# Kernel optimization log

Hardware: AMD Instinct MI355X
Metric: run time of the kernel (lower is better)

## Reference

```python
import jax, jax.numpy as jnp
import numpy as np

NUM_HEADS = 16
HEAD_DIM = 64  # hidden 1024 / 16 heads


def setup_inputs() -> dict:
    key = jax.random.key(0)
    ks = jax.random.split(key, 4)
    B, S, D = 2, 2048, 1024
    scale = 1.0 / np.sqrt(D)
    return {
        "hidden_states": jax.random.normal(ks[0], (B, S, D), jnp.float32),
        "Wq": jax.random.normal(ks[1], (D, D), jnp.float32) * scale,
        "bq": jnp.zeros((D,), jnp.float32),
        "Wk": jax.random.normal(ks[2], (D, D), jnp.float32) * scale,
        "bk": jnp.zeros((D,), jnp.float32),
        "Wv": jax.random.normal(ks[3], (D, D), jnp.float32) * scale,
        "bv": jnp.zeros((D,), jnp.float32),
    }


def _split_heads(x):
    B, S, D = x.shape
    return x.reshape(B, S, NUM_HEADS, HEAD_DIM).transpose(0, 2, 1, 3)  # [B,H,S,dh]


def reference(hidden_states, Wq, bq, Wk, bk, Wv, bv):
    q = _split_heads(hidden_states @ Wq + bq)
    k = _split_heads(hidden_states @ Wk + bk)
    v = _split_heads(hidden_states @ Wv + bv)
    scores = jnp.einsum("bhqd,bhkd->bhqk", q, k) / jnp.sqrt(
        jnp.asarray(HEAD_DIM, hidden_states.dtype))
    probs = jax.nn.softmax(scores, axis=-1)  # dropout is identity in eval mode
    ctx = jnp.einsum("bhqk,bhkd->bhqd", probs, v)
    B, H, S, dh = ctx.shape
    return ctx.transpose(0, 2, 1, 3).reshape(B, S, H * dh)
```

## Files before the change

kernel.cpp:

```cpp
#include <hip/hip_runtime.h>
#include <hip/hip_bf16.h>


typedef __attribute__((ext_vector_type(8))) short bf16x8;
typedef __attribute__((ext_vector_type(4))) float f32x4;
typedef __attribute__((ext_vector_type(4))) int int4v;

#define MFMA16(A, B, C) __builtin_amdgcn_mfma_f32_16x16x32_bf16((A), (B), (C), 0, 0, 0)

#if __has_builtin(__builtin_amdgcn_exp2f)
#define EXP2(x) __builtin_amdgcn_exp2f(x)
#else
#define EXP2(x) exp2f(x)
#endif

static __device__ __forceinline__ unsigned short f2bf(float f) {
    union { float f; unsigned int u; } v;
    v.f = f;
    return (unsigned short)((v.u + 0x8000u) >> 16);
}

static __device__ __forceinline__ void gload_lds16(const void* g, void* l) {
    __builtin_amdgcn_global_load_lds(
        (const __attribute__((address_space(1))) void*)g,
        (__attribute__((address_space(3))) void*)l, 16, 0, 0);
}

__global__ __launch_bounds__(256) void cast_hs(const float* __restrict__ in,
                                               unsigned short* __restrict__ out) {
    const size_t flat = ((size_t)blockIdx.x * 256 + threadIdx.x) * 8;
    const int m = (int)(flat >> 10);
    const int k = (int)(flat & 1023);
    float4 a0 = *reinterpret_cast<const float4*>(in + flat);
    float4 a1 = *reinterpret_cast<const float4*>(in + flat + 4);
    unsigned short t[8];
    t[0] = f2bf(a0.x); t[1] = f2bf(a0.y); t[2] = f2bf(a0.z); t[3] = f2bf(a0.w);
    t[4] = f2bf(a1.x); t[5] = f2bf(a1.y); t[6] = f2bf(a1.z); t[7] = f2bf(a1.w);
    const int csw = (((k >> 3) & 7) ^ (m & 7)) << 3;
    *reinterpret_cast<int4v*>(out + (size_t)m * 1024 + (k & ~63) + csw) =
        *reinterpret_cast<int4v*>(t);
}

__global__ __launch_bounds__(256) void transpose_cast_w(
    const float* __restrict__ W0, const float* __restrict__ W1,
    const float* __restrict__ W2, unsigned short* __restrict__ Wt) {
    __shared__ float Ts[64][65];
    const float* W = (blockIdx.z == 0) ? W0 : (blockIdx.z == 1) ? W1 : W2;
    unsigned short* O = Wt + (size_t)blockIdx.z * 1048576;

    const int t  = threadIdx.x;
    const int k0 = blockIdx.y * 64;
    const int n0 = blockIdx.x * 64;

    {
        const int kr = t >> 2, nc = (t & 3) * 16;
        const float* p = W + (size_t)(k0 + kr) * 1024 + n0 + nc;
        float4 r0 = *reinterpret_cast<const float4*>(p);
        float4 r1 = *reinterpret_cast<const float4*>(p + 4);
        float4 r2 = *reinterpret_cast<const float4*>(p + 8);
        float4 r3 = *reinterpret_cast<const float4*>(p + 12);
        float* d = &Ts[kr][nc];
        d[0]=r0.x; d[1]=r0.y; d[2]=r0.z; d[3]=r0.w;
        d[4]=r1.x; d[5]=r1.y; d[6]=r1.z; d[7]=r1.w;
        d[8]=r2.x; d[9]=r2.y; d[10]=r2.z; d[11]=r2.w;
        d[12]=r3.x; d[13]=r3.y; d[14]=r3.z; d[15]=r3.w;
    }
    __syncthreads();
    {
        const int nr = t >> 2, kc = (t & 3) * 16;
        unsigned short tmp[16];
#pragma unroll
        for (int i = 0; i < 16; i++) tmp[i] = f2bf(Ts[kc + i][nr]);
        unsigned short* base = O + (size_t)(n0 + nr) * 1024 + k0;
        const int c0 = ((kc >> 3) ^ (nr & 7)) & 7;
        const int c1 = (((kc >> 3) + 1) ^ (nr & 7)) & 7;
        *reinterpret_cast<int4v*>(base + c0 * 8) = *reinterpret_cast<int4v*>(&tmp[0]);
        *reinterpret_cast<int4v*>(base + c1 * 8) = *reinterpret_cast<int4v*>(&tmp[8]);
    }
}

__global__ __launch_bounds__(256) void qkv_gemm_dma(
    const unsigned short* __restrict__ hsb,
    const unsigned short* __restrict__ Wt,
    const float* __restrict__ b0, const float* __restrict__ b1,
    const float* __restrict__ b2,
    unsigned short* __restrict__ Qo,
    unsigned short* __restrict__ Ko,
    unsigned short* __restrict__ Vto)
{
    __shared__ unsigned short As[128][64];
    __shared__ unsigned short Bs[128][64];

    const int z = blockIdx.z;
    const unsigned short* W = Wt + (size_t)z * 1048576;
    const float* bias = (z == 0) ? b0 : (z == 1) ? b1 : b2;

    const int tid  = threadIdx.x;
    const int lane = tid & 63;
    const int w    = tid >> 6;
    const int l15  = lane & 15;
    const int quad = lane >> 4;
    const int m0   = blockIdx.y * 128;
    const int n0   = blockIdx.x * 128;
    const int wm   = (w >> 1) * 64;
    const int wn   = (w & 1) * 64;

    const int drow = lane >> 3;
    const int dcol = (lane & 7) * 8;

    f32x4 acc[4][4];
#pragma unroll
    for (int i = 0; i < 4; i++)
#pragma unroll
        for (int j = 0; j < 4; j++)
            acc[i][j] = (f32x4){0.f, 0.f, 0.f, 0.f};

    const int l7 = l15 & 7;

    for (int k0 = 0; k0 < 1024; k0 += 64) {
        __syncthreads();
#pragma unroll
        for (int p = 0; p < 4; p++) {
            const int seg = w * 4 + p;
            gload_lds16(hsb + (size_t)(m0 + seg * 8 + drow) * 1024 + k0 + dcol,
                        &As[seg * 8][0]);
            gload_lds16(W   + (size_t)(n0 + seg * 8 + drow) * 1024 + k0 + dcol,
                        &Bs[seg * 8][0]);
        }
        __syncthreads();

#pragma unroll
        for (int kk = 0; kk < 64; kk += 32) {
            const int csw = ((((kk >> 3) + quad) ^ l7) & 7) * 8;
            bf16x8 af[4], bfr[4];
#pragma unroll
            for (int i = 0; i < 4; i++)
                af[i] = *reinterpret_cast<const bf16x8*>(&As[wm + i * 16 + l15][csw]);
#pragma unroll
            for (int j = 0; j < 4; j++)
                bfr[j] = *reinterpret_cast<const bf16x8*>(&Bs[wn + j * 16 + l15][csw]);
#pragma unroll
            for (int i = 0; i < 4; i++)
#pragma unroll
                for (int j = 0; j < 4; j++)
                    acc[i][j] = MFMA16(af[i], bfr[j], acc[i][j]);
        }
    }

    if (z == 0) {
        const float qs = 0.18033688f;
#pragma unroll
        for (int i = 0; i < 4; i++) {
            const int mbase = m0 + wm + i * 16 + quad * 4;
#pragma unroll
            for (int j = 0; j < 4; j++) {
                const int n = n0 + wn + j * 16 + l15;
                const int h = n >> 6, d = n & 63;
                const float bn = bias[n];
#pragma unroll
                for (int r = 0; r < 4; r++) {
                    const int mm = mbase + r;
                    const int b = mm >> 11, s = mm & 2047;
                    Qo[(((size_t)(b * 16 + h) * 2048 + s) * 64) + d] =
                        f2bf((acc[i][j][r] + bn) * qs);
                }
            }
        }
    } else if (z == 1) {
#pragma unroll
        for (int i = 0; i < 4; i++) {
            const int mbase = m0 + wm + i * 16 + quad * 4;
#pragma unroll
            for (int j = 0; j < 4; j++) {
                const int n = n0 + wn + j * 16 + l15;
                const int h = n >> 6, d = n & 63;
                const float bn = bias[n];
#pragma unroll
                for (int r = 0; r < 4; r++) {
                    const int mm = mbase + r;
                    const int b = mm >> 11, s = mm & 2047;
                    const int dsw = ((((d >> 3) ^ (s & 7)) & 7) << 3) | (d & 7);
                    Ko[(((size_t)(b * 16 + h) * 2048 + s) * 64) + dsw] =
                        f2bf(acc[i][j][r] + bn);
                }
            }
        }
    } else {
#pragma unroll
        for (int i = 0; i < 4; i++) {
            const int mbase = m0 + wm + i * 16 + quad * 4;
            const int b = mbase >> 11, s0 = mbase & 2047;
#pragma unroll
            for (int j = 0; j < 4; j++) {
                const int n = n0 + wn + j * 16 + l15;
                const int h = n >> 6, d = n & 63;
                const float bn = bias[n];
                ushort4 v4;
                v4.x = f2bf(acc[i][j][0] + bn);
                v4.y = f2bf(acc[i][j][1] + bn);
                v4.z = f2bf(acc[i][j][2] + bn);
                v4.w = f2bf(acc[i][j][3] + bn);
                const int cs  = (s0 & 63) >> 3;
                const int ssw = (s0 & ~63) | (((cs ^ (d & 7)) & 7) << 3) | (s0 & 7);
                *reinterpret_cast<ushort4*>(
                    Vto + ((size_t)(b * 16 + h) * 64 + d) * 2048 + ssw) = v4;
            }
        }
    }
}

__global__ __launch_bounds__(256) void attn4(
    const unsigned short* __restrict__ Qg,
    const unsigned short* __restrict__ Kg,
    const unsigned short* __restrict__ Vtg,
    float* __restrict__ out)
{
    __shared__ unsigned short Ks[128][64];
    __shared__ unsigned short Vs[64][128];
    __shared__ unsigned short Ps[4][16][66];

    const int tid  = threadIdx.x;
    const int lane = tid & 63;
    const int w    = tid >> 6;
    const int l15  = lane & 15;
    const int quad = lane >> 4;

    const int q0 = blockIdx.x * 64;
    const int h  = blockIdx.y;
    const int b  = blockIdx.z;
    const size_t base = (size_t)(b * 16 + h) * 2048 * 64;
    const unsigned short* Qh  = Qg  + base;
    const unsigned short* Kh  = Kg  + base;
    const unsigned short* Vth = Vtg + base;

    bf16x8 qf[2];
#pragma unroll
    for (int ks = 0; ks < 2; ks++)
        qf[ks] = *reinterpret_cast<const bf16x8*>(
            Qh + (size_t)(q0 + w * 16 + l15) * 64 + ks * 32 + quad * 8);

    f32x4 o[4];
#pragma unroll
    for (int t = 0; t < 4; t++) o[t] = (f32x4){0.f, 0.f, 0.f, 0.f};
    float rsum[4] = {0.f, 0.f, 0.f, 0.f};

    const int c0 = (((quad + 0) ^ (l15 & 7)) & 7) * 8;
    const int c1 = (((quad + 4) ^ (l15 & 7)) & 7) * 8;

    for (int kt = 0; kt < 16; kt++) {
        __syncthreads();
#pragma unroll
        for (int p = 0; p < 4; p++) {
            const int seg = w * 4 + p;
            gload_lds16(Kh + (size_t)kt * 8192 +
                            (size_t)(seg * 8 + (lane >> 3)) * 64 + (lane & 7) * 8,
                        &Ks[seg * 8][0]);
            gload_lds16(Vth + (size_t)(seg * 4 + (lane >> 4)) * 2048 +
                            kt * 128 + (lane & 15) * 8,
                        &Vs[seg * 4][0]);
        }
        __syncthreads();

#pragma unroll
        for (int u = 0; u < 2; u++) {
#pragma unroll
            for (int t = 0; t < 4; t++) {
                f32x4 sc = (f32x4){0.f, 0.f, 0.f, 0.f};
                {
                    bf16x8 kf = *reinterpret_cast<const bf16x8*>(
                        &Ks[u * 64 + t * 16 + l15][c0]);
                    sc = MFMA16(qf[0], kf, sc);
                }
                {
                    bf16x8 kf = *reinterpret_cast<const bf16x8*>(
                        &Ks[u * 64 + t * 16 + l15][c1]);
                    sc = MFMA16(qf[1], kf, sc);
                }
#pragma unroll
                for (int r = 0; r < 4; r++) {
                    const float p = EXP2(sc[r]);
                    rsum[r] += p;
                    Ps[w][quad * 4 + r][t * 16 + l15] = f2bf(p);
                }
            }

            __builtin_amdgcn_wave_barrier();

            bf16x8 pf[2];
#pragma unroll
            for (int ks = 0; ks < 2; ks++)
                pf[ks] = *reinterpret_cast<const bf16x8*>(
                    &Ps[w][l15][ks * 32 + quad * 8]);
#pragma unroll
            for (int t = 0; t < 4; t++) {
                {
                    bf16x8 vf = *reinterpret_cast<const bf16x8*>(
                        &Vs[t * 16 + l15][u * 64 + c0]);
                    o[t] = MFMA16(pf[0], vf, o[t]);
                }
                {
                    bf16x8 vf = *reinterpret_cast<const bf16x8*>(
                        &Vs[t * 16 + l15][u * 64 + c1]);
                    o[t] = MFMA16(pf[1], vf, o[t]);
                }
            }
            __builtin_amdgcn_wave_barrier();
        }
    }

#pragma unroll
    for (int off = 1; off < 16; off <<= 1)
#pragma unroll
        for (int r = 0; r < 4; r++)
            rsum[r] += __shfl_xor(rsum[r], off, 64);

#pragma unroll
    for (int t = 0; t < 4; t++) {
#pragma unroll
        for (int r = 0; r < 4; r++) {
            const int q = q0 + w * 16 + quad * 4 + r;
            const size_t oidx = (((size_t)b * 2048 + q) * 16 + h) * 64 + t * 16 + l15;
            out[oidx] = o[t][r] / rsum[r];
        }
    }
}

__global__ void fill_sentinel(float* out, int n, float pat) {
    int i = blockIdx.x * blockDim.x + threadIdx.x;
    if (i < n) out[i] = pat;
}

extern "C" void kernel_launch(void* const* d_in, const int* in_sizes, int n_in,
                              void* d_out, int out_size, void* d_ws, size_t ws_size,
                              hipStream_t stream) {
    const size_t n_hs  = (size_t)4096 * 1024;
    const size_t n_w   = (size_t)1024 * 1024;
    const size_t n_qkv = n_hs;
    const size_t need = (n_hs + 3 * n_w + 3 * n_qkv) * sizeof(unsigned short);

    bool order_ok = (n_in == 7) &&
        in_sizes[0] == 4194304 &&
        in_sizes[1] == 1048576 && in_sizes[2] == 1024 &&
        in_sizes[3] == 1048576 && in_sizes[4] == 1024 &&
        in_sizes[5] == 1048576 && in_sizes[6] == 1024;
    if (!order_ok || out_size != 4194304) {
        fill_sentinel<<<(out_size + 255) / 256, 256, 0, stream>>>(
            (float*)d_out, out_size, 4.0f);
        return;
    }
    if (ws_size < need) {
        fill_sentinel<<<(out_size + 255) / 256, 256, 0, stream>>>(
            (float*)d_out, out_size, 2.0f);
        return;
    }

    const float* hs = (const float*)d_in[0];
    const float* Wq = (const float*)d_in[1];
    const float* bq = (const float*)d_in[2];
    const float* Wk = (const float*)d_in[3];
    const float* bk = (const float*)d_in[4];
    const float* Wv = (const float*)d_in[5];
    const float* bv = (const float*)d_in[6];

    unsigned short* hsb = (unsigned short*)d_ws;
    unsigned short* Wt  = hsb + n_hs;
    unsigned short* Q   = Wt + 3 * n_w;
    unsigned short* K   = Q + n_qkv;
    unsigned short* Vt  = K + n_qkv;

    cast_hs<<<2048, 256, 0, stream>>>(hs, hsb);
    transpose_cast_w<<<dim3(16, 16, 3), 256, 0, stream>>>(Wq, Wk, Wv, Wt);

    dim3 g1(8, 32, 3);
    qkv_gemm_dma<<<g1, dim3(256), 0, stream>>>(hsb, Wt, bq, bk, bv, Q, K, Vt);

    dim3 g2(32, 16, 2);
    attn4<<<g2, dim3(256), 0, stream>>>(Q, K, Vt, (float*)d_out);
}
```

Before: 204.8 us.

## Double-buffer K/V tiles in attention kernel to overlap loads with compute

The attention kernel moves from single-buffered 128-key tiles to double-buffered 64-key tiles. The next tile's global-to-LDS DMA is issued before computing on the current buffer, so memory latency overlaps MFMA and exp work. This uses smaller tiles and the same LDS footprint, but needs more iterations and barriers. It also relies on the DMA completing before the following __syncthreads without an explicit vmcnt wait.

```diff
diff --git a/kernel.cpp b/kernel.cpp
--- a/kernel.cpp
+++ b/kernel.cpp
@@ -209,14 +209,14 @@
     }
 }
 
-__global__ __launch_bounds__(256) void attn4(
+__global__ __launch_bounds__(256) void attn5(
     const unsigned short* __restrict__ Qg,
     const unsigned short* __restrict__ Kg,
     const unsigned short* __restrict__ Vtg,
     float* __restrict__ out)
 {
-    __shared__ unsigned short Ks[128][64];
-    __shared__ unsigned short Vs[64][128];
+    __shared__ unsigned short Ks[2][64][64];
+    __shared__ unsigned short Vs[2][64][64];
     __shared__ unsigned short Ps[4][16][66];
 
     const int tid  = threadIdx.x;
@@ -233,6 +233,9 @@
     const unsigned short* Kh  = Kg  + base;
     const unsigned short* Vth = Vtg + base;
 
+    const int drow = lane >> 3;
+    const int dcol = (lane & 7) * 8;
+
     bf16x8 qf[2];
 #pragma unroll
     for (int ks = 0; ks < 2; ks++)
@@ -247,66 +250,75 @@
     const int c0 = (((quad + 0) ^ (l15 & 7)) & 7) * 8;
     const int c1 = (((quad + 4) ^ (l15 & 7)) & 7) * 8;
 
-    for (int kt = 0; kt < 16; kt++) {
+#define STAGE(kt, bb)                                                          \
+    {                                                                          \
+        _Pragma("unroll")                                                      \
+        for (int p = 0; p < 2; p++) {                                          \
+            const int seg = w * 2 + p;                                         \
+            gload_lds16(Kh + (size_t)(kt) * 4096 +                             \
+                            (size_t)(seg * 8 + drow) * 64 + dcol,              \
+                        &Ks[bb][seg * 8][0]);                                  \
+            gload_lds16(Vth + (size_t)(seg * 8 + drow) * 2048 + (kt) * 64 +    \
+                            dcol,                                              \
+                        &Vs[bb][seg * 8][0]);                                  \
+        }                                                                      \
+    }
+
+#define COMPUTE(bb)                                                            \
+    {                                                                          \
+        _Pragma("unroll")                                                      \
+        for (int t = 0; t < 4; t++) {                                          \
+            f32x4 sc = (f32x4){0.f, 0.f, 0.f, 0.f};                            \
+            {                                                                  \
+                bf16x8 kf = *reinterpret_cast<const bf16x8*>(                  \
+                    &Ks[bb][t * 16 + l15][c0]);                                \
+                sc = MFMA16(qf[0], kf, sc);                                    \
+            }                                                                  \
+            {                                                                  \
+                bf16x8 kf = *reinterpret_cast<const bf16x8*>(                  \
+                    &Ks[bb][t * 16 + l15][c1]);                                \
+                sc = MFMA16(qf[1], kf, sc);                                    \
+            }                                                                  \
+            _Pragma("unroll")                                                  \
+            for (int r = 0; r < 4; r++) {                                      \
+                const float p = EXP2(sc[r]);                                   \
+                rsum[r] += p;                                                  \
+                Ps[w][quad * 4 + r][t * 16 + l15] = f2bf(p);                   \
+            }                                                                  \
+        }                                                                      \
+        __builtin_amdgcn_wave_barrier();                                       \
+        bf16x8 pf[2];                                                          \
+        _Pragma("unroll")                                                      \
+        for (int ks = 0; ks < 2; ks++)                                         \
+            pf[ks] = *reinterpret_cast<const bf16x8*>(                         \
+                &Ps[w][l15][ks * 32 + quad * 8]);                              \
+        _Pragma("unroll")                                                      \
+        for (int t = 0; t < 4; t++) {                                          \
+            {                                                                  \
+                bf16x8 vf = *reinterpret_cast<const bf16x8*>(                  \
+                    &Vs[bb][t * 16 + l15][c0]);                                \
+                o[t] = MFMA16(pf[0], vf, o[t]);                                \
+            }                                                                  \
+            {                                                                  \
+                bf16x8 vf = *reinterpret_cast<const bf16x8*>(                  \
+                    &Vs[bb][t * 16 + l15][c1]);                                \
+                o[t] = MFMA16(pf[1], vf, o[t]);                                \
+            }                                                                  \
+        }                                                                      \
+        __builtin_amdgcn_wave_barrier();                                       \
+    }
+
+    STAGE(0, 0);
+    for (int kt = 0; kt < 32; kt += 2) {
         __syncthreads();
-#pragma unroll
-        for (int p = 0; p < 4; p++) {
-            const int seg = w * 4 + p;
-            gload_lds16(Kh + (size_t)kt * 8192 +
-                            (size_t)(seg * 8 + (lane >> 3)) * 64 + (lane & 7) * 8,
-                        &Ks[seg * 8][0]);
-            gload_lds16(Vth + (size_t)(seg * 4 + (lane >> 4)) * 2048 +
-                            kt * 128 + (lane & 15) * 8,
-                        &Vs[seg * 4][0]);
-        }
+        if (kt + 1 < 32) STAGE(kt + 1, 1);
+        COMPUTE(0);
         __syncthreads();
-
-#pragma unroll
-        for (int u = 0; u < 2; u++) {
-#pragma unroll
-            for (int t = 0; t < 4; t++) {
-                f32x4 sc = (f32x4){0.f, 0.f, 0.f, 0.f};
-                {
-                    bf16x8 kf = *reinterpret_cast<const bf16x8*>(
-                        &Ks[u * 64 + t * 16 + l15][c0]);
-                    sc = MFMA16(qf[0], kf, sc);
-                }
-                {
-                    bf16x8 kf = *reinterpret_cast<const bf16x8*>(
-                        &Ks[u * 64 + t * 16 + l15][c1]);
-                    sc = MFMA16(qf[1], kf, sc);
-                }
-#pragma unroll
-                for (int r = 0; r < 4; r++) {
-                    const float p = EXP2(sc[r]);
-                    rsum[r] += p;
-                    Ps[w][quad * 4 + r][t * 16 + l15] = f2bf(p);
-                }
-            }
-
-            __builtin_amdgcn_wave_barrier();
-
-            bf16x8 pf[2];
-#pragma unroll
-            for (int ks = 0; ks < 2; ks++)
-                pf[ks] = *reinterpret_cast<const bf16x8*>(
-                    &Ps[w][l15][ks * 32 + quad * 8]);
-#pragma unroll
-            for (int t = 0; t < 4; t++) {
-                {
-                    bf16x8 vf = *reinterpret_cast<const bf16x8*>(
-                        &Vs[t * 16 + l15][u * 64 + c0]);
-                    o[t] = MFMA16(pf[0], vf, o[t]);
-                }
-                {
-                    bf16x8 vf = *reinterpret_cast<const bf16x8*>(
-                        &Vs[t * 16 + l15][u * 64 + c1]);
-                    o[t] = MFMA16(pf[1], vf, o[t]);
-                }
-            }
-            __builtin_amdgcn_wave_barrier();
-        }
-    }
+        if (kt + 2 < 32) STAGE(kt + 2, 0);
+        COMPUTE(1);
+    }
+#undef STAGE
+#undef COMPUTE
 
 #pragma unroll
     for (int off = 1; off < 16; off <<= 1)
@@ -375,5 +387,5 @@
     qkv_gemm_dma<<<g1, dim3(256), 0, stream>>>(hsb, Wt, bq, bk, bv, Q, K, Vt);
 
     dim3 g2(32, 16, 2);
-    attn4<<<g2, dim3(256), 0, stream>>>(Q, K, Vt, (float*)d_out);
-}
+    attn5<<<g2, dim3(256), 0, stream>>>(Q, K, Vt, (float*)d_out);
+}
```

After: 205.8 us. No clear change (+0.5%).
